# Optimization experiments

Measured on AMD Instinct MI355X. Metric: run time of the kernel, lower is better.

The kernel has to match this reference:

```python
import jax, jax.numpy as jnp
import numpy as np

NUM_L, NUM_W = 10, 10  # num_points_lw


def _local_coords():
    # torch.cartesian_prod(linspace_l, linspace_w) -> (P, 2), l varies slowest
    l = jnp.linspace(-0.5, 0.5, NUM_L)
    w = jnp.linspace(-0.5, 0.5, NUM_W)
    L, W = jnp.meshgrid(l, w, indexing='ij')
    return jnp.stack([L.reshape(-1), W.reshape(-1)], axis=-1)  # (P, 2)


def setup_inputs() -> dict:
    key = jax.random.key(0)
    k1, k2, k3 = jax.random.split(key, 3)
    B, N, T, H, W = 32, 8, 52, 224, 224
    # trajectory states (x, y, vel, yaw, acc, yawvel); positions ~ tens of meters
    x = jax.random.normal(k1, (B, N, T, 6), dtype=jnp.float32) * 5.0
    drivable_map = (jax.random.uniform(k2, (B, H, W)) < 0.7).astype(jnp.float32)
    # realistic vehicle extents (length, width, height)
    extent = jnp.tile(jnp.array([4.5, 2.0, 1.7], jnp.float32), (B, 1)) \
             + 0.2 * jax.random.uniform(k3, (B, 3), dtype=jnp.float32)
    # 2 px/m raster transform centered in the map
    rfa = jnp.array([[2.0, 0.0, W / 2.0], [0.0, 2.0, H / 2.0], [0.0, 0.0, 1.0]],
                    dtype=jnp.float32)
    raster_from_agent = jnp.broadcast_to(rfa, (B, 3, 3))
    return {'x': x, 'drivable_map': drivable_map, 'extent': extent,
            'raster_from_agent': raster_from_agent}


def _forward(x, drivable_map, extent, raster_from_agent):
    B, N, T, _ = x.shape
    _, H, W = drivable_map.shape
    lc = _local_coords()                      # (P, 2)
    P = lc.shape[0]
    M = B * N * T

    traj = x.reshape(M, 6)
    pos = traj[:, :2]                          # (M, 2)
    yaw = traj[:, 3:4]                         # (M, 1)
    lw = jnp.broadcast_to(extent[:, None, None, :], (B, N, T, 3)).reshape(M, 3)[:, :2]
    diag_len = jnp.sqrt(jnp.sum(lw * lw, axis=-1))  # (M,)
    rfa = jnp.broadcast_to(raster_from_agent[:, None, None], (B, N, T, 3, 3)).reshape(M, 3, 3)

    # gen_agt_coords: scale local box grid, rotate, translate
    pts = lc[None, :, :] * lw[:, None, :]      # (M, P, 2)
    s = jnp.sin(yaw)[..., None]                # (M, 1, 1)
    c = jnp.cos(yaw)[..., None]
    rotM = jnp.concatenate([jnp.concatenate([c, s], axis=-1),
                            jnp.concatenate([-s, c], axis=-1)], axis=-2)  # (M, 2, 2)
    agt_pts = pts @ rotM + pos[:, None, :]     # (M, P, 2) agent frame
    # transform_points_tensor: p_pix = R @ p + t (homogeneous 3x3)
    pix = jnp.einsum('mpj,mij->mpi', agt_pts, rfa[:, :2, :2]) + rfa[:, None, :2, 2]
    pix = pix.reshape(B, N, T, P, 2).astype(jnp.int32)   # .long() truncation
    px = jnp.clip(pix[..., 0], 0, W - 1)
    py = jnp.clip(pix[..., 1], 0, H - 1)

    # batch_detect_off_road: gather map values at pixel coords, off-road = 1 - drivable
    drv = jax.vmap(lambda m, ix, iy: m[iy, ix])(drivable_map, px, py)  # (B, N, T, P)
    offroad = 1.0 - drv
    coll = jnp.isclose(offroad, jnp.float32(1.0)).reshape(M, P)  # (M, P) bool

    per_step = jnp.sum(coll, axis=-1)
    overlap = ~((per_step == 0) | (per_step == P))               # (M,) bool

    # pairwise distances (torch.cdist); 2nd copy detached
    a = agt_pts
    b = jax.lax.stop_gradient(agt_pts)
    d2 = (jnp.sum(a * a, -1)[:, :, None] + jnp.sum(b * b, -1)[:, None, :]
          - 2.0 * jnp.einsum('mpd,mqd->mpq', a, b))
    d2 = jnp.maximum(d2, 0.0)
    pos_mask = d2 > 0.0
    dist = jnp.where(pos_mask, jnp.sqrt(jnp.where(pos_mask, d2, 1.0)), 0.0)

    # rows of off-road points -> inf so min is over on-road points
    dist = jnp.where(coll[:, :, None], jnp.inf, dist)
    min_d = jnp.min(dist, axis=1)                                 # (M, P)
    loss_all = 1.0 - min_d / diag_len[:, None]
    loss_off = jnp.where(coll, loss_all, 0.0)
    row_loss = jnp.sum(loss_off, axis=-1)                          # (M,)
    row_loss = jnp.where(overlap, row_loss, 0.0)
    return row_loss.reshape(B, N, T).sum(-1)                       # (B, N)


def reference(x, drivable_map, extent, raster_from_agent):
    return _forward(x, drivable_map, extent, raster_from_agent)
```

## Files before the change

### kernel.cpp

```cpp
#include <hip/hip_runtime.h>
#include <math.h>

#define BB 32
#define NN 8
#define TT 52
#define HH 224
#define WW 224
#define PP 100
#define NWAVE 16

__device__ __forceinline__ float rlane_f(float v, int l) {
    return __int_as_float(__builtin_amdgcn_readlane(__float_as_int(v), l));
}

__global__ __launch_bounds__(NWAVE * 64) void mapcoll_fused(
    const float* __restrict__ x,
    const float* __restrict__ dmap,
    const float* __restrict__ extent,
    const float* __restrict__ rfa,
    float* __restrict__ out)
{
    const int bn   = blockIdx.x;
    const int b    = bn >> 3;
    const int lane = threadIdx.x & 63;
    const int wvu  = __builtin_amdgcn_readfirstlane((int)(threadIdx.x >> 6));

    __shared__ float s_part[NWAVE];

    const float lwx = extent[b * 3 + 0];
    const float lwy = extent[b * 3 + 1];
    const float inv_diag = 1.0f / sqrtf(lwx * lwx + lwy * lwy);
    const float r00 = rfa[b*9+0], r01 = rfa[b*9+1], r02 = rfa[b*9+2];
    const float r10 = rfa[b*9+3], r11 = rfa[b*9+4], r12 = rfa[b*9+5];
    const float* __restrict__ map_b = dmap + (size_t)b * (HH * WW);
    const float sx  = lwx * (1.0f / 9.0f);
    const float sy  = lwy * (1.0f / 9.0f);
    const float sy2 = sy * sy;

    float ppx = 0.0f, ppy = 0.0f, psn = 0.0f, pcs = 1.0f;
    if (lane < TT) {
        const int base = bn * TT * 6 + lane * 6;
        const float2 p2 = *reinterpret_cast<const float2*>(x + base);
        ppx = p2.x; ppy = p2.y;
        const float yw = x[base + 3];
        psn = __sinf(yw);
        pcs = __cosf(yw);
    }

    const int iA = lane / 10, jA = lane - iA * 10;
    const int pB = lane + 64;
    const int iB = pB / 10,   jB = pB - iB * 10;
    const float p0A = (-0.5f + (float)iA * (1.0f/9.0f)) * lwx;
    const float p1A = (-0.5f + (float)jA * (1.0f/9.0f)) * lwy;
    const float p0B = (-0.5f + (float)iB * (1.0f/9.0f)) * lwx;
    const float p1B = (-0.5f + (float)jB * (1.0f/9.0f)) * lwy;
    const bool hasB = (lane < PP - 64);

    const int kn = (wvu < 4) ? 4 : 3;
    const int t0 = (wvu < 4) ? (wvu * 4) : (16 + (wvu - 4) * 3);

    float vA[4], vB[4];
    #pragma unroll
    for (int k = 0; k < 4; ++k) {
        vA[k] = 1.0f;
        vB[k] = 1.0f;
        if (k < kn) {
            const int t = t0 + k;
            const float posx = rlane_f(ppx, t);
            const float posy = rlane_f(ppy, t);
            const float sn   = rlane_f(psn, t);
            const float cs   = rlane_f(pcs, t);
            const float axA = p0A * cs - p1A * sn + posx;
            const float ayA = p0A * sn + p1A * cs + posy;
            {
                const float fx = axA * r00 + ayA * r01 + r02;
                const float fy = axA * r10 + ayA * r11 + r12;
                int ix = (int)fx, iy = (int)fy;
                ix = ix < 0 ? 0 : (ix > WW - 1 ? WW - 1 : ix);
                iy = iy < 0 ? 0 : (iy > HH - 1 ? HH - 1 : iy);
                vA[k] = map_b[iy * WW + ix];
            }
            if (hasB) {
                const float axB = p0B * cs - p1B * sn + posx;
                const float ayB = p0B * sn + p1B * cs + posy;
                const float fx = axB * r00 + ayB * r01 + r02;
                const float fy = axB * r10 + ayB * r11 + r12;
                int ix = (int)fx, iy = (int)fy;
                ix = ix < 0 ? 0 : (ix > WW - 1 ? WW - 1 : ix);
                iy = iy < 0 ? 0 : (iy > HH - 1 ? HH - 1 : iy);
                vB[k] = map_b[iy * WW + ix];
            }
        }
    }

    float acc = 0.0f;
    #pragma unroll
    for (int k = 0; k < 4; ++k) {
        if (k >= kn) continue;
        const int clA = (vA[k] == 0.0f) ? 1 : 0;
        const int clB = (vB[k] == 0.0f) ? 1 : 0;
        const unsigned long long cmA = __ballot(clA);
        const unsigned long long cmB = __ballot(clB);
        const int ncoll = __popcll(cmA) + __popcll(cmB);
        if (ncoll == 0 || ncoll == PP) continue;

        const unsigned long long fA = ~cmA;
        const unsigned long long fB = (~cmB) & ((1ull << 36) - 1ull);
        unsigned rows[10], revs[10];
        #pragma unroll
        for (int r = 0; r < 6; ++r) rows[r] = (unsigned)((fA >> (10 * r)) & 0x3FFull);
        rows[6] = (unsigned)(((fA >> 60) | (fB << 4)) & 0x3FFull);
        #pragma unroll
        for (int r = 7; r < 10; ++r) rows[r] = (unsigned)((fB >> (10 * r - 64)) & 0x3FFull);
        #pragma unroll
        for (int r = 0; r < 10; ++r) revs[r] = __brev(rows[r]) >> 22;

        {
            const int invj = 9 - jA;
            float di = (float)iA * sx;
            float mind2 = 1e30f;
            #pragma unroll
            for (int r = 0; r < 10; ++r) {
                const unsigned t = (rows[r] >> jA) | (revs[r] >> invj) | (1u << 25);
                const unsigned d = __builtin_ctz(t);
                mind2 = fminf(mind2, fmaf(di, di, (float)(d * d) * sy2));
                di -= sx;
            }
            acc += clA ? (1.0f - sqrtf(mind2) * inv_diag) : 0.0f;
        }
        {
            const int invj = 9 - jB;
            float di = (float)iB * sx;
            float mind2 = 1e30f;
            #pragma unroll
            for (int r = 0; r < 10; ++r) {
                const unsigned t = (rows[r] >> jB) | (revs[r] >> invj) | (1u << 25);
                const unsigned d = __builtin_ctz(t);
                mind2 = fminf(mind2, fmaf(di, di, (float)(d * d) * sy2));
                di -= sx;
            }
            acc += clB ? (1.0f - sqrtf(mind2) * inv_diag) : 0.0f;
        }
    }

    #pragma unroll
    for (int off = 32; off > 0; off >>= 1) acc += __shfl_down(acc, off);
    if (lane == 0) s_part[wvu] = acc;
    __syncthreads();
    if (threadIdx.x < 64) {
        float v = (lane < NWAVE) ? s_part[lane] : 0.0f;
        v += __shfl_down(v, 8);
        v += __shfl_down(v, 4);
        v += __shfl_down(v, 2);
        v += __shfl_down(v, 1);
        if (lane == 0) out[bn] = v;
    }
}

extern "C" void kernel_launch(void* const* d_in, const int* in_sizes, int n_in,
                              void* d_out, int out_size, void* d_ws, size_t ws_size,
                              hipStream_t stream) {
    const float* x      = (const float*)d_in[0];
    const float* dmap   = (const float*)d_in[1];
    const float* extent = (const float*)d_in[2];
    const float* rfa    = (const float*)d_in[3];
    float* out = (float*)d_out;

    mapcoll_fused<<<BB * NN, NWAVE * 64, 0, stream>>>(x, dmap, extent, rfa, out);
}
```

Measured before the change: 13.47 us.

## Split each (b,n) across two blocks and combine halves via tagged atomic exchange

Doubles the grid so each block handles 26 of the 52 timesteps for one (b,n) pair, giving each wave at most two steps instead of four. The two partial sums are combined through a workspace slot: each block atomically exchanges a magic-tagged value, and whichever block arrives second writes the output and resets the slot. The map gathers are also moved inside the per-step loop, and the A and B distance searches are interleaved in one loop. This relies on the workspace not happening to contain the magic tag at start, and adds an atomic round-trip per output.

```diff
diff --git a/kernel.cpp b/kernel.cpp
--- a/kernel.cpp
+++ b/kernel.cpp
@@ -8,19 +8,25 @@
 #define WW 224
 #define PP 100
 #define NWAVE 16
+#define TPB 26
+#define MAGICHI 0x5A5A5A5AULL
+#define CLEAN   0xAAAAAAAAAAAAAAAAULL
 
 __device__ __forceinline__ float rlane_f(float v, int l) {
     return __int_as_float(__builtin_amdgcn_readlane(__float_as_int(v), l));
 }
 
-__global__ __launch_bounds__(NWAVE * 64) void mapcoll_fused(
+__global__ __launch_bounds__(NWAVE * 64, 8) void mapcoll_fused(
     const float* __restrict__ x,
     const float* __restrict__ dmap,
     const float* __restrict__ extent,
     const float* __restrict__ rfa,
+    unsigned long long* __restrict__ ws,
     float* __restrict__ out)
 {
-    const int bn   = blockIdx.x;
+    const int bid  = blockIdx.x;
+    const int bn   = bid >> 1;
+    const int half = bid & 1;
     const int b    = bn >> 3;
     const int lane = threadIdx.x & 63;
     const int wvu  = __builtin_amdgcn_readfirstlane((int)(threadIdx.x >> 6));
@@ -38,8 +44,8 @@
     const float sy2 = sy * sy;
 
     float ppx = 0.0f, ppy = 0.0f, psn = 0.0f, pcs = 1.0f;
-    if (lane < TT) {
-        const int base = bn * TT * 6 + lane * 6;
+    if (lane < TPB) {
+        const int base = (bn * TT + half * TPB + lane) * 6;
         const float2 p2 = *reinterpret_cast<const float2*>(x + base);
         ppx = p2.x; ppy = p2.y;
         const float yw = x[base + 3];
@@ -50,55 +56,50 @@
     const int iA = lane / 10, jA = lane - iA * 10;
     const int pB = lane + 64;
     const int iB = pB / 10,   jB = pB - iB * 10;
+    const int invjA = 9 - jA, invjB = 9 - jB;
     const float p0A = (-0.5f + (float)iA * (1.0f/9.0f)) * lwx;
     const float p1A = (-0.5f + (float)jA * (1.0f/9.0f)) * lwy;
     const float p0B = (-0.5f + (float)iB * (1.0f/9.0f)) * lwx;
     const float p1B = (-0.5f + (float)jB * (1.0f/9.0f)) * lwy;
     const bool hasB = (lane < PP - 64);
 
-    const int kn = (wvu < 4) ? 4 : 3;
-    const int t0 = (wvu < 4) ? (wvu * 4) : (16 + (wvu - 4) * 3);
-
-    float vA[4], vB[4];
-    #pragma unroll
-    for (int k = 0; k < 4; ++k) {
-        vA[k] = 1.0f;
-        vB[k] = 1.0f;
-        if (k < kn) {
-            const int t = t0 + k;
-            const float posx = rlane_f(ppx, t);
-            const float posy = rlane_f(ppy, t);
-            const float sn   = rlane_f(psn, t);
-            const float cs   = rlane_f(pcs, t);
-            const float axA = p0A * cs - p1A * sn + posx;
-            const float ayA = p0A * sn + p1A * cs + posy;
-            {
-                const float fx = axA * r00 + ayA * r01 + r02;
-                const float fy = axA * r10 + ayA * r11 + r12;
-                int ix = (int)fx, iy = (int)fy;
-                ix = ix < 0 ? 0 : (ix > WW - 1 ? WW - 1 : ix);
-                iy = iy < 0 ? 0 : (iy > HH - 1 ? HH - 1 : iy);
-                vA[k] = map_b[iy * WW + ix];
-            }
-            if (hasB) {
-                const float axB = p0B * cs - p1B * sn + posx;
-                const float ayB = p0B * sn + p1B * cs + posy;
-                const float fx = axB * r00 + ayB * r01 + r02;
-                const float fy = axB * r10 + ayB * r11 + r12;
-                int ix = (int)fx, iy = (int)fy;
-                ix = ix < 0 ? 0 : (ix > WW - 1 ? WW - 1 : ix);
-                iy = iy < 0 ? 0 : (iy > HH - 1 ? HH - 1 : iy);
-                vB[k] = map_b[iy * WW + ix];
-            }
-        }
-    }
+    const int kn = (wvu < 10) ? 2 : 1;
+    const int t0 = (wvu < 10) ? (wvu * 2) : (20 + (wvu - 10));
 
     float acc = 0.0f;
     #pragma unroll
-    for (int k = 0; k < 4; ++k) {
+    for (int k = 0; k < 2; ++k) {
         if (k >= kn) continue;
-        const int clA = (vA[k] == 0.0f) ? 1 : 0;
-        const int clB = (vB[k] == 0.0f) ? 1 : 0;
+        const int t = t0 + k;
+        const float posx = rlane_f(ppx, t);
+        const float posy = rlane_f(ppy, t);
+        const float sn   = rlane_f(psn, t);
+        const float cs   = rlane_f(pcs, t);
+
+        const float axA = p0A * cs - p1A * sn + posx;
+        const float ayA = p0A * sn + p1A * cs + posy;
+        float vAv, vBv = 1.0f;
+        {
+            const float fx = axA * r00 + ayA * r01 + r02;
+            const float fy = axA * r10 + ayA * r11 + r12;
+            int ix = (int)fx, iy = (int)fy;
+            ix = ix < 0 ? 0 : (ix > WW - 1 ? WW - 1 : ix);
+            iy = iy < 0 ? 0 : (iy > HH - 1 ? HH - 1 : iy);
+            vAv = map_b[iy * WW + ix];
+        }
+        if (hasB) {
+            const float axB = p0B * cs - p1B * sn + posx;
+            const float ayB = p0B * sn + p1B * cs + posy;
+            const float fx = axB * r00 + ayB * r01 + r02;
+            const float fy = axB * r10 + ayB * r11 + r12;
+            int ix = (int)fx, iy = (int)fy;
+            ix = ix < 0 ? 0 : (ix > WW - 1 ? WW - 1 : ix);
+            iy = iy < 0 ? 0 : (iy > HH - 1 ? HH - 1 : iy);
+            vBv = map_b[iy * WW + ix];
+        }
+
+        const int clA = (vAv == 0.0f) ? 1 : 0;
+        const int clB = (vBv == 0.0f) ? 1 : 0;
         const unsigned long long cmA = __ballot(clA);
         const unsigned long long cmB = __ballot(clB);
         const int ncoll = __popcll(cmA) + __popcll(cmB);
@@ -115,32 +116,22 @@
         #pragma unroll
         for (int r = 0; r < 10; ++r) revs[r] = __brev(rows[r]) >> 22;
 
-        {
-            const int invj = 9 - jA;
-            float di = (float)iA * sx;
-            float mind2 = 1e30f;
-            #pragma unroll
-            for (int r = 0; r < 10; ++r) {
-                const unsigned t = (rows[r] >> jA) | (revs[r] >> invj) | (1u << 25);
-                const unsigned d = __builtin_ctz(t);
-                mind2 = fminf(mind2, fmaf(di, di, (float)(d * d) * sy2));
-                di -= sx;
-            }
-            acc += clA ? (1.0f - sqrtf(mind2) * inv_diag) : 0.0f;
+        float mA = 1e30f, mB = 1e30f;
+        float diA = (float)iA * sx;
+        float diB = (float)iB * sx;
+        #pragma unroll
+        for (int r = 0; r < 10; ++r) {
+            const unsigned tA = (rows[r] >> jA) | (revs[r] >> invjA) | (1u << 25);
+            const unsigned tB = (rows[r] >> jB) | (revs[r] >> invjB) | (1u << 25);
+            const unsigned dA = __builtin_ctz(tA);
+            const unsigned dB = __builtin_ctz(tB);
+            mA = fminf(mA, fmaf(diA, diA, (float)(dA * dA) * sy2));
+            mB = fminf(mB, fmaf(diB, diB, (float)(dB * dB) * sy2));
+            diA -= sx;
+            diB -= sx;
         }
-        {
-            const int invj = 9 - jB;
-            float di = (float)iB * sx;
-            float mind2 = 1e30f;
-            #pragma unroll
-            for (int r = 0; r < 10; ++r) {
-                const unsigned t = (rows[r] >> jB) | (revs[r] >> invj) | (1u << 25);
-                const unsigned d = __builtin_ctz(t);
-                mind2 = fminf(mind2, fmaf(di, di, (float)(d * d) * sy2));
-                di -= sx;
-            }
-            acc += clB ? (1.0f - sqrtf(mind2) * inv_diag) : 0.0f;
-        }
+        acc += clA ? (1.0f - sqrtf(mA) * inv_diag) : 0.0f;
+        acc += clB ? (1.0f - sqrtf(mB) * inv_diag) : 0.0f;
     }
 
     #pragma unroll
@@ -153,7 +144,18 @@
         v += __shfl_down(v, 4);
         v += __shfl_down(v, 2);
         v += __shfl_down(v, 1);
-        if (lane == 0) out[bn] = v;
+        if (lane == 0) {
+            const unsigned long long tagged =
+                (MAGICHI << 32) | (unsigned long long)__float_as_uint(v);
+            const unsigned long long old = __hip_atomic_exchange(
+                &ws[bn], tagged, __ATOMIC_ACQ_REL, __HIP_MEMORY_SCOPE_AGENT);
+            if ((old >> 32) == MAGICHI) {
+                const float other = __uint_as_float((unsigned)(old & 0xFFFFFFFFull));
+                out[bn] = v + other;
+                __hip_atomic_store(&ws[bn], CLEAN,
+                                   __ATOMIC_RELEASE, __HIP_MEMORY_SCOPE_AGENT);
+            }
+        }
     }
 }
 
@@ -165,6 +167,7 @@
     const float* extent = (const float*)d_in[2];
     const float* rfa    = (const float*)d_in[3];
     float* out = (float*)d_out;
+    unsigned long long* ws = (unsigned long long*)d_ws;
 
-    mapcoll_fused<<<BB * NN, NWAVE * 64, 0, stream>>>(x, dmap, extent, rfa, out);
+    mapcoll_fused<<<BB * NN * 2, NWAVE * 64, 0, stream>>>(x, dmap, extent, rfa, ws, out);
 }
```

After: 22.31 us. +65.6%, slower.

## Precompute per-point row distance in LDS and fold raster transform into per-step affine

Applied to the files above, without the earlier changes.

Each lane now computes its own in-row nearest free-cell distance once, writes it to a per-wave LDS table, and then reads 10 table entries per point instead of recomputing ctz/bit-reverse across all 10 rows. The raster transform is composed with the rotation per timestep into six affine coefficients, so each point needs two FMA chains. The gather and distance phases are merged into one loop. The cost is extra LDS traffic, a wave barrier per step, and more registers for the precomputed row offsets.

```diff
diff --git a/kernel.cpp b/kernel.cpp
--- a/kernel.cpp
+++ b/kernel.cpp
@@ -25,6 +25,7 @@
     const int lane = threadIdx.x & 63;
     const int wvu  = __builtin_amdgcn_readfirstlane((int)(threadIdx.x >> 6));
 
+    __shared__ float s_w[NWAVE][128];
     __shared__ float s_part[NWAVE];
 
     const float lwx = extent[b * 3 + 0];
@@ -37,109 +38,116 @@
     const float sy  = lwy * (1.0f / 9.0f);
     const float sy2 = sy * sy;
 
-    float ppx = 0.0f, ppy = 0.0f, psn = 0.0f, pcs = 1.0f;
+    float u00 = 0.f, u01 = 0.f, u0c = 0.f, u10 = 0.f, u11 = 0.f, u1c = 0.f;
     if (lane < TT) {
-        const int base = bn * TT * 6 + lane * 6;
+        const int base = (bn * TT + lane) * 6;
         const float2 p2 = *reinterpret_cast<const float2*>(x + base);
-        ppx = p2.x; ppy = p2.y;
         const float yw = x[base + 3];
-        psn = __sinf(yw);
-        pcs = __cosf(yw);
+        const float sn = __sinf(yw), cs = __cosf(yw);
+        u00 = cs * r00 + sn * r01;
+        u01 = cs * r01 - sn * r00;
+        u0c = p2.x * r00 + p2.y * r01 + r02;
+        u10 = cs * r10 + sn * r11;
+        u11 = cs * r11 - sn * r10;
+        u1c = p2.x * r10 + p2.y * r11 + r12;
     }
 
     const int iA = lane / 10, jA = lane - iA * 10;
     const int pB = lane + 64;
     const int iB = pB / 10,   jB = pB - iB * 10;
+    const bool hasB = (lane < PP - 64);
     const float p0A = (-0.5f + (float)iA * (1.0f/9.0f)) * lwx;
     const float p1A = (-0.5f + (float)jA * (1.0f/9.0f)) * lwy;
     const float p0B = (-0.5f + (float)iB * (1.0f/9.0f)) * lwx;
     const float p1B = (-0.5f + (float)jB * (1.0f/9.0f)) * lwy;
-    const bool hasB = (lane < PP - 64);
+
+    const int shA  = (10 * iA) & 63;
+    const int sGA  = (10 * iA - 60) < 0 ? 0 : (10 * iA - 60);
+    const int sGB  = ((10 * iB - 60) & 63);
+    const int rshA = 31 - jA;
+    const int rshB = 31 - jB;
+
+    float di2A[10], di2B[10];
+    #pragma unroll
+    for (int r = 0; r < 10; ++r) {
+        const float dA = (float)(iA - r) * sx; di2A[r] = dA * dA;
+        const float dB = (float)(iB - r) * sx; di2B[r] = dB * dB;
+    }
+
+    float* wtab = &s_w[wvu][0];
+    const unsigned MARK = 1u << 25;
 
     const int kn = (wvu < 4) ? 4 : 3;
     const int t0 = (wvu < 4) ? (wvu * 4) : (16 + (wvu - 4) * 3);
 
-    float vA[4], vB[4];
+    float acc = 0.0f;
     #pragma unroll
     for (int k = 0; k < 4; ++k) {
-        vA[k] = 1.0f;
-        vB[k] = 1.0f;
         if (k < kn) {
             const int t = t0 + k;
-            const float posx = rlane_f(ppx, t);
-            const float posy = rlane_f(ppy, t);
-            const float sn   = rlane_f(psn, t);
-            const float cs   = rlane_f(pcs, t);
-            const float axA = p0A * cs - p1A * sn + posx;
-            const float ayA = p0A * sn + p1A * cs + posy;
+            const float a00 = rlane_f(u00, t), a01 = rlane_f(u01, t), a0c = rlane_f(u0c, t);
+            const float a10 = rlane_f(u10, t), a11 = rlane_f(u11, t), a1c = rlane_f(u1c, t);
+
+            float vAv, vBv = 1.0f;
             {
-                const float fx = axA * r00 + ayA * r01 + r02;
-                const float fy = axA * r10 + ayA * r11 + r12;
+                const float fx = fmaf(p0A, a00, fmaf(p1A, a01, a0c));
+                const float fy = fmaf(p0A, a10, fmaf(p1A, a11, a1c));
                 int ix = (int)fx, iy = (int)fy;
                 ix = ix < 0 ? 0 : (ix > WW - 1 ? WW - 1 : ix);
                 iy = iy < 0 ? 0 : (iy > HH - 1 ? HH - 1 : iy);
-                vA[k] = map_b[iy * WW + ix];
+                vAv = map_b[iy * WW + ix];
             }
             if (hasB) {
-                const float axB = p0B * cs - p1B * sn + posx;
-                const float ayB = p0B * sn + p1B * cs + posy;
-                const float fx = axB * r00 + ayB * r01 + r02;
-                const float fy = axB * r10 + ayB * r11 + r12;
+                const float fx = fmaf(p0B, a00, fmaf(p1B, a01, a0c));
+                const float fy = fmaf(p0B, a10, fmaf(p1B, a11, a1c));
                 int ix = (int)fx, iy = (int)fy;
                 ix = ix < 0 ? 0 : (ix > WW - 1 ? WW - 1 : ix);
                 iy = iy < 0 ? 0 : (iy > HH - 1 ? HH - 1 : iy);
-                vB[k] = map_b[iy * WW + ix];
+                vBv = map_b[iy * WW + ix];
             }
-        }
-    }
 
-    float acc = 0.0f;
-    #pragma unroll
-    for (int k = 0; k < 4; ++k) {
-        if (k >= kn) continue;
-        const int clA = (vA[k] == 0.0f) ? 1 : 0;
-        const int clB = (vB[k] == 0.0f) ? 1 : 0;
-        const unsigned long long cmA = __ballot(clA);
-        const unsigned long long cmB = __ballot(clB);
-        const int ncoll = __popcll(cmA) + __popcll(cmB);
-        if (ncoll == 0 || ncoll == PP) continue;
+            const int clA = (vAv == 0.0f) ? 1 : 0;
+            const int clB = (vBv == 0.0f) ? 1 : 0;
+            const unsigned long long cmA = __ballot(clA);
+            const unsigned long long cmB = __ballot(clB);
+            const int ncoll = __popcll(cmA) + __popcll(cmB);
+            if (ncoll != 0 && ncoll != PP) {
+                const unsigned long long fA = ~cmA;
+                const unsigned long long fB = (~cmB) & ((1ull << 36) - 1ull);
+                const unsigned long long G  = (fA >> 60) | (fB << 4);
 
-        const unsigned long long fA = ~cmA;
-        const unsigned long long fB = (~cmB) & ((1ull << 36) - 1ull);
-        unsigned rows[10], revs[10];
-        #pragma unroll
-        for (int r = 0; r < 6; ++r) rows[r] = (unsigned)((fA >> (10 * r)) & 0x3FFull);
-        rows[6] = (unsigned)(((fA >> 60) | (fB << 4)) & 0x3FFull);
-        #pragma unroll
-        for (int r = 7; r < 10; ++r) rows[r] = (unsigned)((fB >> (10 * r - 64)) & 0x3FFull);
-        #pragma unroll
-        for (int r = 0; r < 10; ++r) revs[r] = __brev(rows[r]) >> 22;
+                {
+                    const unsigned loA = (unsigned)(fA >> shA);
+                    const unsigned gA  = (unsigned)(G  >> sGA);
+                    const unsigned m10 = ((iA < 6) ? loA : gA) & 0x3FFu;
+                    const unsigned tt  = (m10 >> jA) | (__brev(m10) >> rshA) | MARK;
+                    const float d  = (float)__builtin_ctz(tt);
+                    const float ds = d * sy;
+                    wtab[lane] = ds * ds;
+                }
+                if (hasB) {
+                    const unsigned m10 = ((unsigned)(G >> sGB)) & 0x3FFu;
+                    const unsigned tt  = (m10 >> jB) | (__brev(m10) >> rshB) | MARK;
+                    const float d  = (float)__builtin_ctz(tt);
+                    const float ds = d * sy;
+                    wtab[lane + 64] = ds * ds;
+                }
+                asm volatile("s_waitcnt lgkmcnt(0)" ::: "memory");
+                __builtin_amdgcn_wave_barrier();
 
-        {
-            const int invj = 9 - jA;
-            float di = (float)iA * sx;
-            float mind2 = 1e30f;
-            #pragma unroll
-            for (int r = 0; r < 10; ++r) {
-                const unsigned t = (rows[r] >> jA) | (revs[r] >> invj) | (1u << 25);
-                const unsigned d = __builtin_ctz(t);
-                mind2 = fminf(mind2, fmaf(di, di, (float)(d * d) * sy2));
-                di -= sx;
+                float mA = 1e30f, mB = 1e30f;
+                #pragma unroll
+                for (int r = 0; r < 10; r += 2) {
+                    const float wA0 = wtab[r * 10 + jA];
+                    const float wA1 = wtab[r * 10 + 10 + jA];
+                    mA = fminf(mA, fminf(di2A[r] + wA0, di2A[r + 1] + wA1));
+                    const float wB0 = wtab[r * 10 + jB];
+                    const float wB1 = wtab[r * 10 + 10 + jB];
+                    mB = fminf(mB, fminf(di2B[r] + wB0, di2B[r + 1] + wB1));
+                }
+                acc += clA ? (1.0f - sqrtf(mA) * inv_diag) : 0.0f;
+                acc += clB ? (1.0f - sqrtf(mB) * inv_diag) : 0.0f;
             }
-            acc += clA ? (1.0f - sqrtf(mind2) * inv_diag) : 0.0f;
-        }
-        {
-            const int invj = 9 - jB;
-            float di = (float)iB * sx;
-            float mind2 = 1e30f;
-            #pragma unroll
-            for (int r = 0; r < 10; ++r) {
-                const unsigned t = (rows[r] >> jB) | (revs[r] >> invj) | (1u << 25);
-                const unsigned d = __builtin_ctz(t);
-                mind2 = fminf(mind2, fmaf(di, di, (float)(d * d) * sy2));
-                di -= sx;
-            }
-            acc += clB ? (1.0f - sqrtf(mind2) * inv_diag) : 0.0f;
         }
     }
 
```

New measurement: 11.07 us. 1.22x faster.
